# Performance work log

Hardware: AMD Instinct MI355X
Metric: run time of the kernel (lower is better)

## Reference

```python
import jax, jax.numpy as jnp
import numpy as np

N_NODES = 4096
N_EDGES = 16384
D_IN = 128
HID = 1024


def _linear_params(key, fan_in, fan_out):
    kw, kb = jax.random.split(key)
    bound = 1.0 / np.sqrt(fan_in)
    W = jax.random.uniform(kw, (fan_in, fan_out), jnp.float32, -bound, bound)
    b = jax.random.uniform(kb, (fan_out,), jnp.float32, -bound, bound)
    return W, b


def setup_inputs() -> dict:
    key = jax.random.key(0)
    ks = jax.random.split(key, 10)
    H = jax.random.normal(ks[0], (N_NODES, D_IN), jnp.float32)
    e = jax.random.uniform(ks[1], (N_NODES,), jnp.float32)
    # true incidence matrices: one-hot source/destination node per edge
    src = jax.random.randint(ks[2], (N_EDGES,), 0, N_NODES)
    dst = jax.random.randint(ks[3], (N_EDGES,), 0, N_NODES)
    Ro = jax.nn.one_hot(src, N_NODES, dtype=jnp.float32)  # [E, N]
    Ri = jax.nn.one_hot(dst, N_NODES, dtype=jnp.float32)  # [E, N]
    W1, b1 = _linear_params(ks[4], 3 * D_IN, HID)
    W2, b2 = _linear_params(ks[5], HID, HID)
    W3, b3 = _linear_params(ks[6], HID, HID // 2)
    W4, b4 = _linear_params(ks[7], HID // 2, HID // 4)
    W5, b5 = _linear_params(ks[8], HID // 4, 1)
    return {"H": H, "Ro": Ro, "Ri": Ri, "e": e,
            "W1": W1, "b1": b1, "W2": W2, "b2": b2, "W3": W3, "b3": b3,
            "W4": W4, "b4": b4, "W5": W5, "b5": b5}


def reference(H, Ro, Ri, e, W1, b1, W2, b2, W3, b3, W4, b4, W5, b5):
    eH = e[:, None] * H                      # [N, D]
    Ho = Ri.T @ (Ro @ eH)                    # aggregate over edges -> [N, D]
    Hi = Ro.T @ (Ri @ eH)                    # [N, D]
    x = jnp.concatenate([Ho, H, Hi], axis=1)  # [N, 3D]
    x = jnp.tanh(x @ W1 + b1)
    x = jnp.tanh(x @ W2 + b2)
    x = jnp.tanh(x @ W3 + b3)
    x = jnp.tanh(x @ W4 + b4)
    return jax.nn.sigmoid(x @ W5 + b5)       # [N, 1]
```

## Files before the change

### kernel.cpp

```cpp
#include <hip/hip_runtime.h>
#include <hip/hip_bf16.h>
#include <math.h>

#define N_NODES 4096
#define N_EDGES 16384
#define D_IN 128
#define HID 1024

typedef short s8v __attribute__((ext_vector_type(8)));
typedef float f4v __attribute__((ext_vector_type(4)));

__device__ __forceinline__ unsigned short f2b(float v) {
    union { float f; unsigned int u; } c; c.f = v;
    unsigned int u = c.u + 0x7fffu + ((c.u >> 16) & 1u);
    return (unsigned short)(u >> 16);
}
__device__ __forceinline__ void glds16(const unsigned short* g, unsigned short* l) {
    __builtin_amdgcn_global_load_lds(
        (const __attribute__((address_space(1))) void*)g,
        (__attribute__((address_space(3))) void*)l, 16, 0, 0);
}

__global__ void zero_counts(int* __restrict__ c) {
    c[blockIdx.x * 256 + threadIdx.x] = 0;
}

__global__ void extract_wt(const float* __restrict__ Ro, const float* __restrict__ Ri,
                           int* __restrict__ src_arr, int* __restrict__ dst_arr,
                           int* __restrict__ counts,
                           const float* __restrict__ W1, unsigned short* __restrict__ wt1,
                           const float* __restrict__ W2, unsigned short* __restrict__ wt2,
                           const float* __restrict__ W3, unsigned short* __restrict__ wt3,
                           const float* __restrict__ W4, unsigned short* __restrict__ wt4) {
    int b = blockIdx.x, t = threadIdx.x;
    if (b < 4096) {
        int edge = (b * 256 + t) >> 6;
        int l = t & 63;
        const f4v* ro4 = (const f4v*)(Ro + (size_t)edge * N_NODES);
        const f4v* ri4 = (const f4v*)(Ri + (size_t)edge * N_NODES);
        int src = -1, dst = -1;
        for (int g = 0; g < 4; ++g) {
            f4v va[4], vb[4];
            bool needA = (src < 0), needB = (dst < 0);
            if (needA) {
#pragma unroll
                for (int i = 0; i < 4; ++i)
                    va[i] = __builtin_nontemporal_load(&ro4[(g * 4 + i) * 64 + l]);
            }
            if (needB) {
#pragma unroll
                for (int i = 0; i < 4; ++i)
                    vb[i] = __builtin_nontemporal_load(&ri4[(g * 4 + i) * 64 + l]);
            }
            if (needA) {
#pragma unroll
                for (int i = 0; i < 4; ++i) {
                    if (src < 0) {
                        f4v v = va[i];
                        bool hit = (v.x != 0.0f) | (v.y != 0.0f) | (v.z != 0.0f) | (v.w != 0.0f);
                        unsigned long long m = __ballot(hit);
                        if (m) {
                            int fl = __ffsll((long long)m) - 1;
                            int idx = 0;
                            if (hit) idx = ((g * 4 + i) * 64 + l) * 4 +
                                           (v.x != 0.0f ? 0 : v.y != 0.0f ? 1 : v.z != 0.0f ? 2 : 3);
                            src = __shfl(idx, fl);
                        }
                    }
                }
            }
            if (needB) {
#pragma unroll
                for (int i = 0; i < 4; ++i) {
                    if (dst < 0) {
                        f4v v = vb[i];
                        bool hit = (v.x != 0.0f) | (v.y != 0.0f) | (v.z != 0.0f) | (v.w != 0.0f);
                        unsigned long long m = __ballot(hit);
                        if (m) {
                            int fl = __ffsll((long long)m) - 1;
                            int idx = 0;
                            if (hit) idx = ((g * 4 + i) * 64 + l) * 4 +
                                           (v.x != 0.0f ? 0 : v.y != 0.0f ? 1 : v.z != 0.0f ? 2 : 3);
                            dst = __shfl(idx, fl);
                        }
                    }
                }
            }
            if (src >= 0 && dst >= 0) break;
        }
        if (l == 0) {
            src_arr[edge] = src;
            dst_arr[edge] = dst;
            atomicAdd(&counts[dst], 1);
            atomicAdd(&counts[4096 + src], 1);
        }
        return;
    }
    int wb = b - 4096;
    const float* W; unsigned short* WT; int K, N, tb;
    if (wb < 384)       { W = W1; WT = wt1; K = 384;  N = 1024; tb = wb; }
    else if (wb < 1408) { W = W2; WT = wt2; K = 1024; N = 1024; tb = wb - 384; }
    else if (wb < 1920) { W = W3; WT = wt3; K = 1024; N = 512;  tb = wb - 1408; }
    else                { W = W4; WT = wt4; K = 512;  N = 256;  tb = wb - 1920; }
    __shared__ float tile[32][33];
    int ntx = N >> 5;
    int tk = tb / ntx, tn = tb - tk * ntx;
    int tr = t >> 5, tc = t & 31;
#pragma unroll
    for (int i = 0; i < 4; ++i)
        tile[tr + i * 8][tc] = W[(size_t)(tk * 32 + tr + i * 8) * N + tn * 32 + tc];
    __syncthreads();
#pragma unroll
    for (int i = 0; i < 4; ++i)
        WT[(size_t)(tn * 32 + tr + i * 8) * K + tk * 32 + tc] = f2b(tile[tc][tr + i * 8]);
}

__global__ __launch_bounds__(1024)
void scan_offsets(const int* __restrict__ counts, int* __restrict__ starts,
                  int* __restrict__ cursors) {
    __shared__ int part[1024];
    int t = threadIdx.x;
    for (int a = 0; a < 2; ++a) {
        const int* c = counts + a * 4096;
        int v[4], s = 0;
#pragma unroll
        for (int i = 0; i < 4; ++i) { v[i] = c[t * 4 + i]; s += v[i]; }
        part[t] = s;
        __syncthreads();
        for (int off = 1; off < 1024; off <<= 1) {
            int x = (t >= off) ? part[t - off] : 0;
            __syncthreads();
            part[t] += x;
            __syncthreads();
        }
        int o = part[t] - s;
#pragma unroll
        for (int i = 0; i < 4; ++i) {
            starts[a * 4096 + t * 4 + i]  = o;
            cursors[a * 4096 + t * 4 + i] = o;
            o += v[i];
        }
        __syncthreads();
    }
}

__global__ void fill_lists(const int* __restrict__ src_arr, const int* __restrict__ dst_arr,
                           int* __restrict__ cursors,
                           int* __restrict__ in_list, int* __restrict__ out_list) {
    int e = blockIdx.x * 256 + threadIdx.x;
    int s = src_arr[e], d = dst_arr[e];
    int p = atomicAdd(&cursors[d], 1);
    in_list[p] = e;
    int p2 = atomicAdd(&cursors[4096 + s], 1);
    out_list[p2] = e;
}

__global__ __launch_bounds__(64)
void gather_a1(const float* __restrict__ H, const float* __restrict__ e_arr,
               const int* __restrict__ src_arr, const int* __restrict__ dst_arr,
               const int* __restrict__ starts, const int* __restrict__ counts,
               const int* __restrict__ in_list, const int* __restrict__ out_list,
               unsigned short* __restrict__ A1) {
    int n = blockIdx.x;
    int l = threadIdx.x;
    bool lo = l < 32;
    int f = (lo ? l : l - 32) * 4;
    int base = lo ? starts[n] : starts[4096 + n];
    int cnt  = lo ? counts[n] : counts[4096 + n];
    const int* list  = lo ? in_list : out_list;
    const int* other = lo ? src_arr : dst_arr;
    f4v acc = {0.f, 0.f, 0.f, 0.f};
    for (int i = 0; i < cnt; ++i) {
        int eidx = list[base + i];
        int node = other[eidx];
        float s = e_arr[node];
        f4v h = *(const f4v*)(H + (size_t)node * 128 + f);
        acc.x += s * h.x; acc.y += s * h.y; acc.z += s * h.z; acc.w += s * h.w;
    }
    ushort4 pk;
    pk.x = f2b(acc.x); pk.y = f2b(acc.y); pk.z = f2b(acc.z); pk.w = f2b(acc.w);
    *(ushort4*)&A1[(size_t)n * 384 + (lo ? 0 : 256) + f] = pk;
    if (lo) {
        f4v h = *(const f4v*)(H + (size_t)n * 128 + f);
        ushort4 ph;
        ph.x = f2b(h.x); ph.y = f2b(h.y); ph.z = f2b(h.z); ph.w = f2b(h.w);
        *(ushort4*)&A1[(size_t)n * 384 + 128 + f] = ph;
    }
}

template<int BM, int BN>
__global__ __launch_bounds__(256)
void gemm_tanh(const unsigned short* __restrict__ A, const unsigned short* __restrict__ BT,
               const float* __restrict__ bias, unsigned short* __restrict__ C,
               int M, int N, int K) {
    constexpr int BK = 32;
    constexpr int MI = BM / 32, NI = BN / 32;
    constexpr int AITER = BM / 64, BITER = BN / 64;
    __shared__ unsigned short As[BM * BK];
    __shared__ unsigned short Bs[BN * BK];
    int t = threadIdx.x;
    int l = t & 63, w = t >> 6;
    int wm = w >> 1, wn = w & 1;
    int q = l >> 4, r16 = l & 15;
    int m0 = blockIdx.y * BM, n0 = blockIdx.x * BN;

    f4v acc[MI][NI] = {};

    for (int k0 = 0; k0 < K; k0 += BK) {
        __syncthreads();
#pragma unroll
        for (int i = 0; i < AITER; ++i) {
            int c = (i * 4 + w) * 64 + l;
            int row = c >> 2, ko = (c & 3) * 8;
            glds16(&A[(size_t)(m0 + row) * K + k0 + ko], &As[c * 8]);
        }
#pragma unroll
        for (int i = 0; i < BITER; ++i) {
            int c = (i * 4 + w) * 64 + l;
            int row = c >> 2, ko = (c & 3) * 8;
            glds16(&BT[(size_t)(n0 + row) * K + k0 + ko], &Bs[c * 8]);
        }
        __syncthreads();
        s8v a[MI], b[NI];
#pragma unroll
        for (int mi = 0; mi < MI; ++mi)
            a[mi] = *(const s8v*)&As[(wm * (BM / 2) + mi * 16 + r16) * BK + q * 8];
#pragma unroll
        for (int ni = 0; ni < NI; ++ni)
            b[ni] = *(const s8v*)&Bs[(wn * (BN / 2) + ni * 16 + r16) * BK + q * 8];
#pragma unroll
        for (int mi = 0; mi < MI; ++mi)
#pragma unroll
            for (int ni = 0; ni < NI; ++ni)
                acc[mi][ni] = __builtin_amdgcn_mfma_f32_16x16x32_bf16(a[mi], b[ni], acc[mi][ni], 0, 0, 0);
    }
#pragma unroll
    for (int mi = 0; mi < MI; ++mi)
#pragma unroll
        for (int ni = 0; ni < NI; ++ni) {
            int col = n0 + wn * (BN / 2) + ni * 16 + r16;
            float bv = bias[col];
#pragma unroll
            for (int r = 0; r < 4; ++r) {
                int row = m0 + wm * (BM / 2) + mi * 16 + q * 4 + r;
                C[(size_t)row * N + col] = f2b(tanhf(acc[mi][ni][r] + bv));
            }
        }
}

__global__ __launch_bounds__(256)
void gemm45(const unsigned short* __restrict__ A, const unsigned short* __restrict__ BT,
            const float* __restrict__ b4, const float* __restrict__ W5,
            const float* __restrict__ b5, float* __restrict__ out) {
    constexpr int BK = 32, K = 512, NN = 256;
    constexpr int NI = 8;
    __shared__ unsigned short As[32 * BK];
    __shared__ unsigned short Bs[NN * BK];
    __shared__ float part[32][2];
    int t = threadIdx.x;
    int l = t & 63, w = t >> 6;
    int wm = w >> 1, wn = w & 1;
    int q = l >> 4, r16 = l & 15;
    int m0 = blockIdx.y * 32;

    f4v acc[NI] = {};

    for (int k0 = 0; k0 < K; k0 += BK) {
        __syncthreads();
        if (w < 2) {
            int c = w * 64 + l;
            int row = c >> 2, ko = (c & 3) * 8;
            glds16(&A[(size_t)(m0 + row) * K + k0 + ko], &As[c * 8]);
        }
#pragma unroll
        for (int i = 0; i < 4; ++i) {
            int c = (i * 4 + w) * 64 + l;
            int row = c >> 2, ko = (c & 3) * 8;
            glds16(&BT[(size_t)row * K + k0 + ko], &Bs[c * 8]);
        }
        __syncthreads();
        s8v a = *(const s8v*)&As[(wm * 16 + r16) * BK + q * 8];
        s8v b[NI];
#pragma unroll
        for (int ni = 0; ni < NI; ++ni)
            b[ni] = *(const s8v*)&Bs[(wn * 128 + ni * 16 + r16) * BK + q * 8];
#pragma unroll
        for (int ni = 0; ni < NI; ++ni)
            acc[ni] = __builtin_amdgcn_mfma_f32_16x16x32_bf16(a, b[ni], acc[ni], 0, 0, 0);
    }

    float partial[4] = {0.f, 0.f, 0.f, 0.f};
#pragma unroll
    for (int ni = 0; ni < NI; ++ni) {
        int col = wn * 128 + ni * 16 + r16;
        float bv = b4[col], wv = W5[col];
#pragma unroll
        for (int r = 0; r < 4; ++r)
            partial[r] += tanhf(acc[ni][r] + bv) * wv;
    }
#pragma unroll
    for (int off = 1; off < 16; off <<= 1)
#pragma unroll
        for (int r = 0; r < 4; ++r)
            partial[r] += __shfl_xor(partial[r], off);
    if (r16 == 0)
#pragma unroll
        for (int r = 0; r < 4; ++r)
            part[wm * 16 + q * 4 + r][wn] = partial[r];
    __syncthreads();
    if (t < 32) {
        float s = part[t][0] + part[t][1] + b5[0];
        out[m0 + t] = 1.0f / (1.0f + expf(-s));
    }
}

extern "C" void kernel_launch(void* const* d_in, const int* in_sizes, int n_in,
                              void* d_out, int out_size, void* d_ws, size_t ws_size,
                              hipStream_t stream) {
    const float* H  = (const float*)d_in[0];
    const float* Ro = (const float*)d_in[1];
    const float* Ri = (const float*)d_in[2];
    const float* e  = (const float*)d_in[3];
    const float* W1 = (const float*)d_in[4];  const float* b1 = (const float*)d_in[5];
    const float* W2 = (const float*)d_in[6];  const float* b2 = (const float*)d_in[7];
    const float* W3 = (const float*)d_in[8];  const float* b3 = (const float*)d_in[9];
    const float* W4 = (const float*)d_in[10]; const float* b4 = (const float*)d_in[11];
    const float* W5 = (const float*)d_in[12]; const float* b5 = (const float*)d_in[13];
    float* out = (float*)d_out;

    char* p = (char*)d_ws;
    auto alloc = [&](size_t bytes) -> void* {
        void* r = (void*)p;
        p += (bytes + 255) & ~(size_t)255;
        return r;
    };
    int* counts   = (int*)alloc(8192 * 4);
    int* starts   = (int*)alloc(8192 * 4);
    int* cursors  = (int*)alloc(8192 * 4);
    int* src_arr  = (int*)alloc(N_EDGES * 4);
    int* dst_arr  = (int*)alloc(N_EDGES * 4);
    int* in_list  = (int*)alloc(N_EDGES * 4);
    int* out_list = (int*)alloc(N_EDGES * 4);
    unsigned short* a1  = (unsigned short*)alloc((size_t)N_NODES * 384 * 2);
    unsigned short* h1  = (unsigned short*)alloc((size_t)N_NODES * HID * 2);
    unsigned short* h2  = (unsigned short*)alloc((size_t)N_NODES * HID * 2);
    unsigned short* h3  = (unsigned short*)alloc((size_t)N_NODES * (HID / 2) * 2);
    unsigned short* wt1 = (unsigned short*)alloc((size_t)HID * 384 * 2);
    unsigned short* wt2 = (unsigned short*)alloc((size_t)HID * HID * 2);
    unsigned short* wt3 = (unsigned short*)alloc((size_t)(HID / 2) * HID * 2);
    unsigned short* wt4 = (unsigned short*)alloc((size_t)(HID / 4) * (HID / 2) * 2);

    zero_counts<<<32, 256, 0, stream>>>(counts);

    extract_wt<<<4096 + 2048, 256, 0, stream>>>(Ro, Ri, src_arr, dst_arr, counts,
                                                W1, wt1, W2, wt2, W3, wt3, W4, wt4);

    scan_offsets<<<1, 1024, 0, stream>>>(counts, starts, cursors);

    fill_lists<<<64, 256, 0, stream>>>(src_arr, dst_arr, cursors, in_list, out_list);

    gather_a1<<<N_NODES, 64, 0, stream>>>(H, e, src_arr, dst_arr, starts, counts,
                                          in_list, out_list, a1);

    gemm_tanh<128, 64><<<dim3(HID / 64, N_NODES / 128), 256, 0, stream>>>(a1, wt1, b1, h1, N_NODES, HID, 384);
    gemm_tanh<128, 64><<<dim3(HID / 64, N_NODES / 128), 256, 0, stream>>>(h1, wt2, b2, h2, N_NODES, HID, HID);
    gemm_tanh<64, 64><<<dim3((HID / 2) / 64, N_NODES / 64), 256, 0, stream>>>(h2, wt3, b3, h3, N_NODES, HID / 2, HID);

    gemm45<<<dim3(1, N_NODES / 32), 256, 0, stream>>>(h3, wt4, b4, W5, b5, out);
}
```

Baseline: 562.7 us.

## Double-buffer GEMM LDS tiles with BK=64, XOR swizzle and vmcnt waits

Reworks the MLP GEMM kernels into a double-buffered pipeline. The next K tile is loaded directly into a second LDS buffer while the current one feeds MFMA, with explicit vmcnt waits and raw barriers replacing __syncthreads. BK doubles to 64 so each barrier covers more MFMAs, and an XOR swizzle on the 16-byte groups is meant to avoid LDS bank conflicts. This doubles LDS use, which may lower occupancy, and correctness depends on the hand-counted vmcnt values.

Measured after the change: 548.0 us. -2.6%, faster.

```diff
diff --git a/kernel.cpp b/kernel.cpp
--- a/kernel.cpp
+++ b/kernel.cpp
@@ -19,6 +19,12 @@
     __builtin_amdgcn_global_load_lds(
         (const __attribute__((address_space(1))) void*)g,
         (__attribute__((address_space(3))) void*)l, 16, 0, 0);
+}
+template<int N> __device__ __forceinline__ void vmcnt_wait() {
+    if constexpr (N == 0)      asm volatile("s_waitcnt vmcnt(0)" ::: "memory");
+    else if constexpr (N == 4) asm volatile("s_waitcnt vmcnt(4)" ::: "memory");
+    else if constexpr (N == 6) asm volatile("s_waitcnt vmcnt(6)" ::: "memory");
+    else if constexpr (N == 9) asm volatile("s_waitcnt vmcnt(9)" ::: "memory");
 }
 
 __global__ void zero_counts(int* __restrict__ c) {
@@ -190,14 +196,14 @@
 
 template<int BM, int BN>
 __global__ __launch_bounds__(256)
-void gemm_tanh(const unsigned short* __restrict__ A, const unsigned short* __restrict__ BT,
-               const float* __restrict__ bias, unsigned short* __restrict__ C,
-               int M, int N, int K) {
-    constexpr int BK = 32;
+void gemm_db(const unsigned short* __restrict__ A, const unsigned short* __restrict__ BT,
+             const float* __restrict__ bias, unsigned short* __restrict__ C,
+             int N, int K) {
+    constexpr int BK = 64;
     constexpr int MI = BM / 32, NI = BN / 32;
-    constexpr int AITER = BM / 64, BITER = BN / 64;
-    __shared__ unsigned short As[BM * BK];
-    __shared__ unsigned short Bs[BN * BK];
+    constexpr int IA = BM / 32, IB = BN / 32, IS = IA + IB;
+    __shared__ unsigned short As[2][BM * BK];
+    __shared__ unsigned short Bs[2][BN * BK];
     int t = threadIdx.x;
     int l = t & 63, w = t >> 6;
     int wm = w >> 1, wn = w & 1;
@@ -206,33 +212,51 @@
 
     f4v acc[MI][NI] = {};
 
+    auto stage = [&](int buf, int k0) {
+#pragma unroll
+        for (int i = 0; i < IA; ++i) {
+            int c = i * 256 + t;
+            int row = c >> 3, g = c & 7, gs = g ^ (row & 7);
+            glds16(&A[(size_t)(m0 + row) * K + k0 + gs * 8], &As[buf][c * 8]);
+        }
+#pragma unroll
+        for (int i = 0; i < IB; ++i) {
+            int c = i * 256 + t;
+            int row = c >> 3, g = c & 7, gs = g ^ (row & 7);
+            glds16(&BT[(size_t)(n0 + row) * K + k0 + gs * 8], &Bs[buf][c * 8]);
+        }
+    };
+
+    stage(0, 0);
+    int cur = 0;
     for (int k0 = 0; k0 < K; k0 += BK) {
-        __syncthreads();
-#pragma unroll
-        for (int i = 0; i < AITER; ++i) {
-            int c = (i * 4 + w) * 64 + l;
-            int row = c >> 2, ko = (c & 3) * 8;
-            glds16(&A[(size_t)(m0 + row) * K + k0 + ko], &As[c * 8]);
-        }
-#pragma unroll
-        for (int i = 0; i < BITER; ++i) {
-            int c = (i * 4 + w) * 64 + l;
-            int row = c >> 2, ko = (c & 3) * 8;
-            glds16(&BT[(size_t)(n0 + row) * K + k0 + ko], &Bs[c * 8]);
-        }
-        __syncthreads();
-        s8v a[MI], b[NI];
-#pragma unroll
-        for (int mi = 0; mi < MI; ++mi)
-            a[mi] = *(const s8v*)&As[(wm * (BM / 2) + mi * 16 + r16) * BK + q * 8];
-#pragma unroll
-        for (int ni = 0; ni < NI; ++ni)
-            b[ni] = *(const s8v*)&Bs[(wn * (BN / 2) + ni * 16 + r16) * BK + q * 8];
-#pragma unroll
-        for (int mi = 0; mi < MI; ++mi)
-#pragma unroll
-            for (int ni = 0; ni < NI; ++ni)
-                acc[mi][ni] = __builtin_amdgcn_mfma_f32_16x16x32_bf16(a[mi], b[ni], acc[mi][ni], 0, 0, 0);
+        if (k0 + BK < K) { stage(cur ^ 1, k0 + BK); vmcnt_wait<IS>(); }
+        else             { vmcnt_wait<0>(); }
+        __builtin_amdgcn_s_barrier();
+        s8v a[MI][2], b[NI][2];
+#pragma unroll
+        for (int mi = 0; mi < MI; ++mi) {
+            int row = wm * (BM / 2) + mi * 16 + r16;
+#pragma unroll
+            for (int kk = 0; kk < 2; ++kk)
+                a[mi][kk] = *(const s8v*)&As[cur][row * 64 + ((((kk << 2) | q)) ^ (row & 7)) * 8];
+        }
+#pragma unroll
+        for (int ni = 0; ni < NI; ++ni) {
+            int row = wn * (BN / 2) + ni * 16 + r16;
+#pragma unroll
+            for (int kk = 0; kk < 2; ++kk)
+                b[ni][kk] = *(const s8v*)&Bs[cur][row * 64 + ((((kk << 2) | q)) ^ (row & 7)) * 8];
+        }
+#pragma unroll
+        for (int kk = 0; kk < 2; ++kk)
+#pragma unroll
+            for (int mi = 0; mi < MI; ++mi)
+#pragma unroll
+                for (int ni = 0; ni < NI; ++ni)
+                    acc[mi][ni] = __builtin_amdgcn_mfma_f32_16x16x32_bf16(a[mi][kk], b[ni][kk], acc[mi][ni], 0, 0, 0);
+        __builtin_amdgcn_s_barrier();
+        cur ^= 1;
     }
 #pragma unroll
     for (int mi = 0; mi < MI; ++mi)
@@ -252,10 +276,10 @@
 void gemm45(const unsigned short* __restrict__ A, const unsigned short* __restrict__ BT,
             const float* __restrict__ b4, const float* __restrict__ W5,
             const float* __restrict__ b5, float* __restrict__ out) {
-    constexpr int BK = 32, K = 512, NN = 256;
+    constexpr int BK = 64, K = 512;
     constexpr int NI = 8;
-    __shared__ unsigned short As[32 * BK];
-    __shared__ unsigned short Bs[NN * BK];
+    __shared__ unsigned short As[2][32 * BK];
+    __shared__ unsigned short Bs[2][256 * BK];
     __shared__ float part[32][2];
     int t = threadIdx.x;
     int l = t & 63, w = t >> 6;
@@ -265,28 +289,47 @@
 
     f4v acc[NI] = {};
 
+    auto stage = [&](int buf, int k0) {
+        {
+            int c = t;
+            int row = c >> 3, g = c & 7, gs = g ^ (row & 7);
+            glds16(&A[(size_t)(m0 + row) * K + k0 + gs * 8], &As[buf][c * 8]);
+        }
+#pragma unroll
+        for (int i = 0; i < 8; ++i) {
+            int c = i * 256 + t;
+            int row = c >> 3, g = c & 7, gs = g ^ (row & 7);
+            glds16(&BT[(size_t)row * K + k0 + gs * 8], &Bs[buf][c * 8]);
+        }
+    };
+
+    stage(0, 0);
+    int cur = 0;
     for (int k0 = 0; k0 < K; k0 += BK) {
-        __syncthreads();
-        if (w < 2) {
-            int c = w * 64 + l;
-            int row = c >> 2, ko = (c & 3) * 8;
-            glds16(&A[(size_t)(m0 + row) * K + k0 + ko], &As[c * 8]);
-        }
-#pragma unroll
-        for (int i = 0; i < 4; ++i) {
-            int c = (i * 4 + w) * 64 + l;
-            int row = c >> 2, ko = (c & 3) * 8;
-            glds16(&BT[(size_t)row * K + k0 + ko], &Bs[c * 8]);
-        }
-        __syncthreads();
-        s8v a = *(const s8v*)&As[(wm * 16 + r16) * BK + q * 8];
-        s8v b[NI];
-#pragma unroll
-        for (int ni = 0; ni < NI; ++ni)
-            b[ni] = *(const s8v*)&Bs[(wn * 128 + ni * 16 + r16) * BK + q * 8];
-#pragma unroll
-        for (int ni = 0; ni < NI; ++ni)
-            acc[ni] = __builtin_amdgcn_mfma_f32_16x16x32_bf16(a, b[ni], acc[ni], 0, 0, 0);
+        if (k0 + BK < K) { stage(cur ^ 1, k0 + BK); vmcnt_wait<9>(); }
+        else             { vmcnt_wait<0>(); }
+        __builtin_amdgcn_s_barrier();
+        s8v a[2], b[NI][2];
+        {
+            int row = wm * 16 + r16;
+#pragma unroll
+            for (int kk = 0; kk < 2; ++kk)
+                a[kk] = *(const s8v*)&As[cur][row * 64 + ((((kk << 2) | q)) ^ (row & 7)) * 8];
+        }
+#pragma unroll
+        for (int ni = 0; ni < NI; ++ni) {
+            int row = wn * 128 + ni * 16 + r16;
+#pragma unroll
+            for (int kk = 0; kk < 2; ++kk)
+                b[ni][kk] = *(const s8v*)&Bs[cur][row * 64 + ((((kk << 2) | q)) ^ (row & 7)) * 8];
+        }
+#pragma unroll
+        for (int kk = 0; kk < 2; ++kk)
+#pragma unroll
+            for (int ni = 0; ni < NI; ++ni)
+                acc[ni] = __builtin_amdgcn_mfma_f32_16x16x32_bf16(a[kk], b[ni][kk], acc[ni], 0, 0, 0);
+        __builtin_amdgcn_s_barrier();
+        cur ^= 1;
     }
 
     float partial[4] = {0.f, 0.f, 0.f, 0.f};
@@ -362,9 +405,9 @@
     gather_a1<<<N_NODES, 64, 0, stream>>>(H, e, src_arr, dst_arr, starts, counts,
                                           in_list, out_list, a1);
 
-    gemm_tanh<128, 64><<<dim3(HID / 64, N_NODES / 128), 256, 0, stream>>>(a1, wt1, b1, h1, N_NODES, HID, 384);
-    gemm_tanh<128, 64><<<dim3(HID / 64, N_NODES / 128), 256, 0, stream>>>(h1, wt2, b2, h2, N_NODES, HID, HID);
-    gemm_tanh<64, 64><<<dim3((HID / 2) / 64, N_NODES / 64), 256, 0, stream>>>(h2, wt3, b3, h3, N_NODES, HID / 2, HID);
+    gemm_db<128, 64><<<dim3(HID / 64, N_NODES / 128), 256, 0, stream>>>(a1, wt1, b1, h1, HID, 384);
+    gemm_db<128, 64><<<dim3(HID / 64, N_NODES / 128), 256, 0, stream>>>(h1, wt2, b2, h2, HID, HID);
+    gemm_db<64, 64><<<dim3((HID / 2) / 64, N_NODES / 64), 256, 0, stream>>>(h2, wt3, b3, h3, HID / 2, HID);
 
     gemm45<<<dim3(1, N_NODES / 32), 256, 0, stream>>>(h3, wt4, b4, W5, b5, out);
 }
```
